# Performance work log

Measured on AMD Instinct MI355X. Metric: run time of the kernel, lower is better.

## Reference

```python
import jax, jax.numpy as jnp
import numpy as np

N_NODES = 16384
N_EDGES = 524288
N_GRAPHS = 256
IN_CH = 128
H_CH = 128   # per-head channels
HEADS = 2
LAYER_DIM = HEADS * H_CH  # 256, concat=True
POOL_DIM = 3 * LAYER_DIM  # 768
OUT_CH = 1
NEG_SLOPE = 0.2


def setup_inputs() -> dict:
    key = jax.random.key(0)
    ks = jax.random.split(key, 20)
    s = lambda k, shape, fan: jax.random.normal(k, shape, jnp.float32) * (1.0 / np.sqrt(fan))
    inp = {
        "x": jax.random.normal(ks[0], (N_NODES, IN_CH), jnp.float32),
        "edge_index": jax.random.randint(ks[1], (2, N_EDGES), 0, N_NODES, jnp.int64),
        "batch": jnp.sort(jax.random.randint(ks[2], (N_NODES,), 0, N_GRAPHS, jnp.int64)),
        # GATv2 layer 1 (in=128)
        "Wl1": s(ks[3], (IN_CH, LAYER_DIM), IN_CH), "Wr1": s(ks[4], (IN_CH, LAYER_DIM), IN_CH),
        "att1": s(ks[5], (HEADS, H_CH), H_CH), "b1": jnp.zeros((LAYER_DIM,), jnp.float32),
        # GATv2 layer 2 (in=256)
        "Wl2": s(ks[6], (LAYER_DIM, LAYER_DIM), LAYER_DIM), "Wr2": s(ks[7], (LAYER_DIM, LAYER_DIM), LAYER_DIM),
        "att2": s(ks[8], (HEADS, H_CH), H_CH), "b2": jnp.zeros((LAYER_DIM,), jnp.float32),
        # GATv2 layer 3 (in=256)
        "Wl3": s(ks[9], (LAYER_DIM, LAYER_DIM), LAYER_DIM), "Wr3": s(ks[10], (LAYER_DIM, LAYER_DIM), LAYER_DIM),
        "att3": s(ks[11], (HEADS, H_CH), H_CH), "b3": jnp.zeros((LAYER_DIM,), jnp.float32),
        # FFN (dropout inactive at eval)
        "fW1": s(ks[12], (POOL_DIM, POOL_DIM), POOL_DIM), "fb1": jnp.zeros((POOL_DIM,), jnp.float32),
        "fW2": s(ks[13], (POOL_DIM, OUT_CH), POOL_DIM), "fb2": jnp.zeros((OUT_CH,), jnp.float32),
    }
    return inp


def _gatv2(x, src, dst, Wl, Wr, att, b):
    """PyG GATv2Conv: per-edge score a . LeakyReLU(Wl x_src + Wr x_dst),
    softmax over incoming edges per destination, weighted scatter-add of Wl x_src."""
    n = x.shape[0]
    xl = (x @ Wl).reshape(n, HEADS, H_CH)  # source messages
    xr = (x @ Wr).reshape(n, HEADS, H_CH)  # target query
    e = jax.nn.leaky_relu(xl[src] + xr[dst], NEG_SLOPE)          # [E,H,C]
    logits = jnp.einsum('ehc,hc->eh', e, att)                    # [E,H]
    m = jax.ops.segment_max(logits, dst, num_segments=n)         # per-dst max (self-loops guarantee nonempty)
    ev = jnp.exp(logits - m[dst])
    denom = jax.ops.segment_sum(ev, dst, num_segments=n)
    alpha = ev / denom[dst]                                       # [E,H]
    out = jax.ops.segment_sum(alpha[..., None] * xl[src], dst, num_segments=n)  # [N,H,C]
    return out.reshape(n, LAYER_DIM) + b


def reference(x, edge_index, batch, Wl1, Wr1, att1, b1, Wl2, Wr2, att2, b2,
              Wl3, Wr3, att3, b3, fW1, fb1, fW2, fb2):
    n = x.shape[0]
    loops = jnp.arange(n, dtype=edge_index.dtype)
    src = jnp.concatenate([edge_index[0], loops])  # add_self_loops=True default
    dst = jnp.concatenate([edge_index[1], loops])
    h1 = _gatv2(x, src, dst, Wl1, Wr1, att1, b1)
    h2 = _gatv2(h1, src, dst, Wl2, Wr2, att2, b2)
    h3 = _gatv2(h2, src, dst, Wl3, Wr3, att3, b3)
    pool = lambda h: jax.ops.segment_sum(h, batch, num_segments=N_GRAPHS)
    h = jnp.concatenate([pool(h1), pool(h2), pool(h3)], axis=1)   # [G,768]
    h = jax.nn.relu(h @ fW1 + fb1)
    return h @ fW2 + fb2                                           # [G,1]
```

## Files before the change

### kernel.cpp

```cpp
#include <hip/hip_runtime.h>

#define NNODES 16384
#define NEDGES 524288
#define NETOT  (NEDGES + NNODES)
#define NGRAPH 256

typedef __attribute__((ext_vector_type(8))) short short8;
typedef __attribute__((ext_vector_type(4))) float f32x4;
typedef __attribute__((ext_vector_type(2))) float f32x2;

__device__ __forceinline__ float b2f(unsigned short u){
  union { unsigned int i; float f; } v; v.i = ((unsigned int)u) << 16; return v.f;
}
__device__ __forceinline__ unsigned short f2b(float f){
  union { float f; unsigned int i; } v; v.f = f;
  unsigned int r = v.i + 0x7FFFu + ((v.i >> 16) & 1u);
  return (unsigned short)(r >> 16);
}
__device__ __forceinline__ f32x2 unpack2(unsigned int u){
  union { unsigned int i; float f; } lo, hi;
  lo.i = u << 16; hi.i = u & 0xFFFF0000u;
  f32x2 r; r[0] = lo.f; r[1] = hi.f; return r;
}

__global__ void __launch_bounds__(256) zero_deg(int* __restrict__ deg){
  deg[blockIdx.x * 256 + threadIdx.x] = 0;
}

__global__ void __launch_bounds__(256) count_deg(const int* __restrict__ ei, int* __restrict__ deg){
  int i = blockIdx.x * 256 + threadIdx.x;
  int d = (i < NEDGES) ? ei[NEDGES + i] : (i - NEDGES);
  atomicAdd(&deg[d], 1);
}

__global__ void __launch_bounds__(256) scan1(const int* __restrict__ deg,
                                             int* __restrict__ incl, int* __restrict__ bsum){
  __shared__ int ws[4];
  const int b = blockIdx.x, t = threadIdx.x, lane = t & 63, w = t >> 6;
  int v = deg[b * 256 + t];
  int x = v;
  #pragma unroll
  for(int o = 1; o < 64; o <<= 1){ int u = __shfl_up(x, o, 64); if(lane >= o) x += u; }
  if(lane == 63) ws[w] = x;
  __syncthreads();
  int add = 0;
  #pragma unroll
  for(int j = 0; j < 4; j++) if(j < w) add += ws[j];
  incl[b * 256 + t] = x + add;
  if(t == 255) bsum[b] = x + add;
}

__global__ void __launch_bounds__(256) scan3(const int* __restrict__ deg, const int* __restrict__ incl,
                                             const int* __restrict__ bsum,
                                             int* __restrict__ row_off, int* __restrict__ cursor){
  __shared__ int boff_s;
  const int b = blockIdx.x, t = threadIdx.x;
  if(t < 64){
    int v = (t < b) ? bsum[t] : 0;
    #pragma unroll
    for(int o = 32; o > 0; o >>= 1) v += __shfl_xor(v, o, 64);
    if(t == 0) boff_s = v;
  }
  __syncthreads();
  const int i = b * 256 + t;
  int inc = incl[i] + boff_s;
  row_off[i + 1] = inc;
  cursor[i] = inc - deg[i];
  if(i == 0) row_off[0] = 0;
}

__global__ void __launch_bounds__(256) fill_csr(const int* __restrict__ ei, int* __restrict__ cursor,
                                                int* __restrict__ col_src){
  int i = blockIdx.x * 256 + threadIdx.x;
  int s, d;
  if(i < NEDGES){ s = ei[i]; d = ei[NEDGES + i]; }
  else          { s = i - NEDGES; d = s; }
  int p = atomicAdd(&cursor[d], 1);
  col_src[p] = s;
}

__global__ void __launch_bounds__(256) prep(const float* __restrict__ x,
                                            const float* __restrict__ Wl1, const float* __restrict__ Wr1,
                                            const float* __restrict__ Wl2, const float* __restrict__ Wr2,
                                            const float* __restrict__ Wl3, const float* __restrict__ Wr3,
                                            unsigned short* __restrict__ xb,
                                            unsigned short* __restrict__ Wt1,
                                            unsigned short* __restrict__ Wt2,
                                            unsigned short* __restrict__ Wt3){
  const int b = blockIdx.x, t = threadIdx.x;
  if(b < 8192){
    int i = b * 256 + t;
    xb[i] = f2b(x[i]);
    return;
  }
  const float *Wl, *Wr; unsigned short* Wt; int K, i;
  if(b < 8192 + 256){ Wl = Wl1; Wr = Wr1; Wt = Wt1; K = 128; i = (b - 8192) * 256 + t; }
  else if(b < 8192 + 256 + 512){ Wl = Wl2; Wr = Wr2; Wt = Wt2; K = 256; i = (b - 8448) * 256 + t; }
  else { Wl = Wl3; Wr = Wr3; Wt = Wt3; K = 256; i = (b - 8960) * 256 + t; }
  int k = i >> 9, c = i & 511;
  float val = (c < 256) ? Wl[(size_t)k * 256 + c] : Wr[(size_t)k * 256 + (c - 256)];
  Wt[(size_t)c * K + k] = f2b(val);
}

template<int K>
__global__ void __launch_bounds__(256) gemm_xw(const unsigned short* __restrict__ A,
                                               const unsigned short* __restrict__ Wt,
                                               unsigned short* __restrict__ Cout){
  __shared__ unsigned short As[128][40];
  __shared__ unsigned short Bs[128][40];
  const int t = threadIdx.x;
  const int rowbase = blockIdx.x * 128;
  const int colbase = blockIdx.y * 128;
  const int wave = t >> 6, lane = t & 63;
  const int lrow = lane & 15, kg = lane >> 4;

  f32x4 acc[2][8] = {};

  for(int kt = 0; kt < K; kt += 32){
    {
      int oct = t & 3, r = t >> 2;
      const unsigned short* ga = A + (size_t)(rowbase + r) * K + kt + oct * 8;
      short8 v0 = *(const short8*)ga;
      short8 v1 = *(const short8*)(ga + 64 * K);
      *(short8*)(&As[r][oct * 8])      = v0;
      *(short8*)(&As[r + 64][oct * 8]) = v1;
    }
    {
      int n = t & 127, kh = (t >> 7) * 16;
      const unsigned short* gw = Wt + (size_t)(colbase + n) * K + kt + kh;
      short8 v0 = *(const short8*)gw;
      short8 v1 = *(const short8*)(gw + 8);
      *(short8*)(&Bs[n][kh])     = v0;
      *(short8*)(&Bs[n][kh + 8]) = v1;
    }
    __syncthreads();
    short8 afrag[2], bfrag[8];
    afrag[0] = *(const short8*)(&As[wave * 32 + lrow][kg * 8]);
    afrag[1] = *(const short8*)(&As[wave * 32 + 16 + lrow][kg * 8]);
    #pragma unroll
    for(int fc = 0; fc < 8; fc++) bfrag[fc] = *(const short8*)(&Bs[fc * 16 + lrow][kg * 8]);
    #pragma unroll
    for(int rf = 0; rf < 2; rf++)
      #pragma unroll
      for(int fc = 0; fc < 8; fc++)
        acc[rf][fc] = __builtin_amdgcn_mfma_f32_16x16x32_bf16(afrag[rf], bfrag[fc], acc[rf][fc], 0, 0, 0);
    __syncthreads();
  }
  #pragma unroll
  for(int rf = 0; rf < 2; rf++)
    #pragma unroll
    for(int fc = 0; fc < 8; fc++)
      #pragma unroll
      for(int r = 0; r < 4; r++){
        int row = rowbase + wave * 32 + rf * 16 + kg * 4 + r;
        int col = colbase + fc * 16 + lrow;
        Cout[(size_t)row * 512 + col] = f2b(acc[rf][fc][r]);
      }
}

__global__ void __launch_bounds__(256) edge_agg(const unsigned short* __restrict__ xlb,
                                                const int* __restrict__ row_off,
                                                const int* __restrict__ col_src,
                                                const float* __restrict__ att,
                                                const float* __restrict__ bias,
                                                unsigned short* __restrict__ hout){
  const int n = (blockIdx.x * 256 + threadIdx.x) >> 6;
  const int lane = threadIdx.x & 63;
  const int eg = lane >> 4;
  const int c0 = (lane & 15) * 16;
  f32x2 xr[8], at[8];
  {
    const unsigned short* xp = xlb + (size_t)n * 512 + 256 + c0;
    uint4 v0 = *(const uint4*)xp;
    uint4 v1 = *(const uint4*)(xp + 8);
    xr[0] = unpack2(v0.x); xr[1] = unpack2(v0.y); xr[2] = unpack2(v0.z); xr[3] = unpack2(v0.w);
    xr[4] = unpack2(v1.x); xr[5] = unpack2(v1.y); xr[6] = unpack2(v1.z); xr[7] = unpack2(v1.w);
    #pragma unroll
    for(int i = 0; i < 8; i++) at[i] = *(const f32x2*)(att + c0 + 2 * i);
  }
  float s = 0.f;
  f32x2 ac[8] = {};
  const int beg = row_off[n], end = row_off[n + 1];
  for(int ch = beg; ch < end; ch += 64){
    int idx = ch + lane;
    int si = (idx < end) ? col_src[idx] : 0;
    int cnt = end - ch; if(cnt > 64) cnt = 64;
    for(int k = 0; k < cnt; k += 4){
      int kk = k + eg;
      int src = __shfl(si, kk);
      const unsigned short* gp = xlb + (size_t)src * 512 + c0;
      uint4 v0 = *(const uint4*)gp;
      uint4 v1 = *(const uint4*)(gp + 8);
      f32x2 x0 = unpack2(v0.x), x1 = unpack2(v0.y), x2 = unpack2(v0.z), x3 = unpack2(v0.w);
      f32x2 x4 = unpack2(v1.x), x5 = unpack2(v1.y), x6 = unpack2(v1.z), x7 = unpack2(v1.w);
      f32x2 e, p2;
      e = x0 + xr[0]; e = __builtin_elementwise_max(e, e * 0.2f); p2  = e * at[0];
      e = x1 + xr[1]; e = __builtin_elementwise_max(e, e * 0.2f); p2 += e * at[1];
      e = x2 + xr[2]; e = __builtin_elementwise_max(e, e * 0.2f); p2 += e * at[2];
      e = x3 + xr[3]; e = __builtin_elementwise_max(e, e * 0.2f); p2 += e * at[3];
      e = x4 + xr[4]; e = __builtin_elementwise_max(e, e * 0.2f); p2 += e * at[4];
      e = x5 + xr[5]; e = __builtin_elementwise_max(e, e * 0.2f); p2 += e * at[5];
      e = x6 + xr[6]; e = __builtin_elementwise_max(e, e * 0.2f); p2 += e * at[6];
      e = x7 + xr[7]; e = __builtin_elementwise_max(e, e * 0.2f); p2 += e * at[7];
      float p = p2[0] + p2[1];
      p += __shfl_xor(p, 1); p += __shfl_xor(p, 2); p += __shfl_xor(p, 4);
      float pe = (kk < cnt) ? __expf(p) : 0.f;
      s += pe;
      f32x2 pe2 = {pe, pe};
      ac[0] += pe2 * x0; ac[1] += pe2 * x1; ac[2] += pe2 * x2; ac[3] += pe2 * x3;
      ac[4] += pe2 * x4; ac[5] += pe2 * x5; ac[6] += pe2 * x6; ac[7] += pe2 * x7;
    }
  }
  s += __shfl_xor(s, 16); s += __shfl_xor(s, 32);
  #pragma unroll
  for(int i = 0; i < 8; i++){
    ac[i][0] += __shfl_xor(ac[i][0], 16); ac[i][0] += __shfl_xor(ac[i][0], 32);
    ac[i][1] += __shfl_xor(ac[i][1], 16); ac[i][1] += __shfl_xor(ac[i][1], 32);
  }
  if(eg == 0){
    float inv = 1.f / s;
    unsigned short o[16];
    #pragma unroll
    for(int i = 0; i < 8; i++){
      o[2 * i]     = f2b(fmaf(ac[i][0], inv, bias[c0 + 2 * i]));
      o[2 * i + 1] = f2b(fmaf(ac[i][1], inv, bias[c0 + 2 * i + 1]));
    }
    unsigned short* hp = hout + (size_t)n * 256 + c0;
    *(uint4*)hp       = *(const uint4*)&o[0];
    *(uint4*)(hp + 8) = *(const uint4*)&o[8];
  }
}

__device__ __forceinline__ int lbound(const int* __restrict__ a, int n, int v){
  int lo = 0, hi = n;
  while(lo < hi){ int mid = (lo + hi) >> 1; if(a[mid] < v) lo = mid + 1; else hi = mid; }
  return lo;
}

__global__ void __launch_bounds__(256) pool_accum(const unsigned short* __restrict__ h,
                                                  const int* __restrict__ batch,
                                                  float* __restrict__ pool, int slot){
  __shared__ float red[8][264];
  const int g = blockIdx.x, t = threadIdx.x;
  const int ng = t >> 5, c0 = (t & 31) * 8;
  const int lo = lbound(batch, NNODES, g);
  const int hi = lbound(batch, NNODES, g + 1);
  f32x2 a0 = {0.f,0.f}, a1 = {0.f,0.f}, a2 = {0.f,0.f}, a3 = {0.f,0.f};
  for(int node = lo + ng; node < hi; node += 8){
    uint4 v = *(const uint4*)(h + (size_t)node * 256 + c0);
    a0 += unpack2(v.x); a1 += unpack2(v.y); a2 += unpack2(v.z); a3 += unpack2(v.w);
  }
  red[ng][c0 + 0] = a0[0]; red[ng][c0 + 1] = a0[1];
  red[ng][c0 + 2] = a1[0]; red[ng][c0 + 3] = a1[1];
  red[ng][c0 + 4] = a2[0]; red[ng][c0 + 5] = a2[1];
  red[ng][c0 + 6] = a3[0]; red[ng][c0 + 7] = a3[1];
  __syncthreads();
  float s = 0.f;
  #pragma unroll
  for(int i = 0; i < 8; i++) s += red[i][t];
  pool[(size_t)g * 768 + slot * 256 + t] = s;
}

__global__ void __launch_bounds__(256) ffn1(const float* __restrict__ pool,
                                            const float* __restrict__ fW1,
                                            const float* __restrict__ fb1,
                                            float* __restrict__ hidden){
  __shared__ float ap[32][65];
  __shared__ float ws[64][33];
  const int t = threadIdx.x;
  const int cb = blockIdx.x * 32;
  const int gb = blockIdx.y * 32;
  const int tc = t & 31, tg = t >> 5;
  float acc[4] = {};
  for(int kc = 0; kc < 768; kc += 64){
    {
      int g_l = t >> 3, j8 = (t & 7) * 8;
      const float* gp = pool + (size_t)(gb + g_l) * 768 + kc + j8;
      #pragma unroll
      for(int i = 0; i < 8; i++) ap[g_l][j8 + i] = gp[i];
    }
    {
      int c_l = t & 31, k0 = (t >> 5) * 8;
      #pragma unroll
      for(int i = 0; i < 8; i++) ws[k0 + i][c_l] = fW1[(size_t)(kc + k0 + i) * 768 + cb + c_l];
    }
    __syncthreads();
    #pragma unroll
    for(int k = 0; k < 64; k++){
      float w = ws[k][tc];
      #pragma unroll
      for(int i = 0; i < 4; i++) acc[i] = fmaf(ap[tg * 4 + i][k], w, acc[i]);
    }
    __syncthreads();
  }
  float b = fb1[cb + tc];
  #pragma unroll
  for(int i = 0; i < 4; i++)
    hidden[(size_t)(gb + tg * 4 + i) * 768 + cb + tc] = fmaxf(acc[i] + b, 0.f);
}

__global__ void __launch_bounds__(256) ffn2(const float* __restrict__ hidden,
                                            const float* __restrict__ fW2,
                                            const float* __restrict__ fb2,
                                            float* __restrict__ out){
  const int g = (blockIdx.x * 256 + threadIdx.x) >> 6;
  const int lane = threadIdx.x & 63;
  float p = 0.f;
  for(int i = lane; i < 768; i += 64) p += hidden[(size_t)g * 768 + i] * fW2[i];
  #pragma unroll
  for(int o = 32; o > 0; o >>= 1) p += __shfl_xor(p, o, 64);
  if(lane == 0) out[g] = p + fb2[0];
}

extern "C" void kernel_launch(void* const* d_in, const int* in_sizes, int n_in,
                              void* d_out, int out_size, void* d_ws, size_t ws_size,
                              hipStream_t stream){
  const float* x    = (const float*)d_in[0];
  const int* ei     = (const int*)d_in[1];
  const int* batch  = (const int*)d_in[2];
  const float* Wl[3]  = {(const float*)d_in[3],  (const float*)d_in[7],  (const float*)d_in[11]};
  const float* Wr[3]  = {(const float*)d_in[4],  (const float*)d_in[8],  (const float*)d_in[12]};
  const float* att[3] = {(const float*)d_in[5],  (const float*)d_in[9],  (const float*)d_in[13]};
  const float* bp[3]  = {(const float*)d_in[6],  (const float*)d_in[10], (const float*)d_in[14]};
  const float* fW1 = (const float*)d_in[15];
  const float* fb1 = (const float*)d_in[16];
  const float* fW2 = (const float*)d_in[17];
  const float* fb2 = (const float*)d_in[18];

  char* ws = (char*)d_ws;
  size_t off = 0;
  auto alloc = [&](size_t sz){ size_t p = off; off += (sz + 255) & ~(size_t)255; return p; };
  int* deg      = (int*)(ws + alloc((size_t)NNODES * 4));
  int* rowoff   = (int*)(ws + alloc((size_t)(NNODES + 1) * 4));
  int* cursor   = (int*)(ws + alloc((size_t)NNODES * 4));
  int* colsrc   = (int*)(ws + alloc((size_t)NETOT * 4));
  int* incl     = (int*)(ws + alloc((size_t)NNODES * 4));
  int* bsum     = (int*)(ws + alloc(64 * 4));
  unsigned short* xb  = (unsigned short*)(ws + alloc((size_t)NNODES * 128 * 2));
  unsigned short* Wt1 = (unsigned short*)(ws + alloc((size_t)512 * 128 * 2));
  unsigned short* Wt2 = (unsigned short*)(ws + alloc((size_t)512 * 256 * 2));
  unsigned short* Wt3 = (unsigned short*)(ws + alloc((size_t)512 * 256 * 2));
  unsigned short* xlb = (unsigned short*)(ws + alloc((size_t)NNODES * 512 * 2));
  unsigned short* hA  = (unsigned short*)(ws + alloc((size_t)NNODES * 256 * 2));
  unsigned short* hB  = (unsigned short*)(ws + alloc((size_t)NNODES * 256 * 2));
  float* pool   = (float*)(ws + alloc((size_t)NGRAPH * 768 * 4));
  float* hidden = (float*)(ws + alloc((size_t)NGRAPH * 768 * 4));

  zero_deg<<<NNODES / 256, 256, 0, stream>>>(deg);
  count_deg<<<NETOT / 256, 256, 0, stream>>>(ei, deg);
  prep<<<8192 + 256 + 512 + 512, 256, 0, stream>>>(x, Wl[0], Wr[0], Wl[1], Wr[1], Wl[2], Wr[2],
                                                   xb, Wt1, Wt2, Wt3);
  scan1<<<NNODES / 256, 256, 0, stream>>>(deg, incl, bsum);
  scan3<<<NNODES / 256, 256, 0, stream>>>(deg, incl, bsum, rowoff, cursor);
  fill_csr<<<NETOT / 256, 256, 0, stream>>>(ei, cursor, colsrc);

  dim3 ggrid(NNODES / 128, 4);

  gemm_xw<128><<<ggrid, 256, 0, stream>>>(xb, Wt1, xlb);
  edge_agg<<<NNODES / 4, 256, 0, stream>>>(xlb, rowoff, colsrc, att[0], bp[0], hA);
  pool_accum<<<NGRAPH, 256, 0, stream>>>(hA, batch, pool, 0);

  gemm_xw<256><<<ggrid, 256, 0, stream>>>(hA, Wt2, xlb);
  edge_agg<<<NNODES / 4, 256, 0, stream>>>(xlb, rowoff, colsrc, att[1], bp[1], hB);
  pool_accum<<<NGRAPH, 256, 0, stream>>>(hB, batch, pool, 1);

  gemm_xw<256><<<ggrid, 256, 0, stream>>>(hB, Wt3, xlb);
  edge_agg<<<NNODES / 4, 256, 0, stream>>>(xlb, rowoff, colsrc, att[2], bp[2], hA);
  pool_accum<<<NGRAPH, 256, 0, stream>>>(hA, batch, pool, 2);

  ffn1<<<dim3(768 / 32, NGRAPH / 32), 256, 0, stream>>>(pool, fW1, fb1, hidden);
  ffn2<<<NGRAPH / 4, 256, 0, stream>>>(hidden, fW2, fb2, (float*)d_out);
}
```

Measured before the change: 286.3 us.

## Split GAT layers per head into compact buffers and fuse pooling into aggregation

The GEMM now writes xl for each head into its own compact 128-wide buffer and xr into a separate buffer. Edge aggregation runs once per head, so each gathered row is 256 bytes and the random-access footprint shrinks, which should improve L2 locality. Pooling is fused into edge_agg through float atomics, and the pool buffer is zeroed inside prep, which removes the pool_accum kernels. The change also adds a prefetch touch of the block's own xl rows, nontemporal loads and stores, and two edges per inner iteration. In exchange it doubles the number of aggregation launches and adds atomic contention on the pool buffer.

```diff
diff --git a/kernel.cpp b/kernel.cpp
--- a/kernel.cpp
+++ b/kernel.cpp
@@ -8,6 +8,7 @@
 typedef __attribute__((ext_vector_type(8))) short short8;
 typedef __attribute__((ext_vector_type(4))) float f32x4;
 typedef __attribute__((ext_vector_type(2))) float f32x2;
+typedef __attribute__((ext_vector_type(4))) unsigned int u32x4;
 
 __device__ __forceinline__ float b2f(unsigned short u){
   union { unsigned int i; float f; } v; v.i = ((unsigned int)u) << 16; return v.f;
@@ -86,11 +87,18 @@
                                             unsigned short* __restrict__ xb,
                                             unsigned short* __restrict__ Wt1,
                                             unsigned short* __restrict__ Wt2,
-                                            unsigned short* __restrict__ Wt3){
+                                            unsigned short* __restrict__ Wt3,
+                                            float* __restrict__ pool){
   const int b = blockIdx.x, t = threadIdx.x;
   if(b < 8192){
     int i = b * 256 + t;
     xb[i] = f2b(x[i]);
+    return;
+  }
+  if(b >= 9472){
+    int i = (b - 9472) * 1024 + t * 4;
+    f32x4 z = {0.f, 0.f, 0.f, 0.f};
+    *(f32x4*)(pool + i) = z;
     return;
   }
   const float *Wl, *Wr; unsigned short* Wt; int K, i;
@@ -105,12 +113,15 @@
 template<int K>
 __global__ void __launch_bounds__(256) gemm_xw(const unsigned short* __restrict__ A,
                                                const unsigned short* __restrict__ Wt,
-                                               unsigned short* __restrict__ Cout){
+                                               unsigned short* __restrict__ xl0,
+                                               unsigned short* __restrict__ xl1,
+                                               unsigned short* __restrict__ xr){
   __shared__ unsigned short As[128][40];
   __shared__ unsigned short Bs[128][40];
   const int t = threadIdx.x;
   const int rowbase = blockIdx.x * 128;
-  const int colbase = blockIdx.y * 128;
+  const int by = blockIdx.y;
+  const int colbase = by * 128;
   const int wave = t >> 6, lane = t & 63;
   const int lrow = lane & 15, kg = lane >> 4;
 
@@ -146,6 +157,10 @@
         acc[rf][fc] = __builtin_amdgcn_mfma_f32_16x16x32_bf16(afrag[rf], bfrag[fc], acc[rf][fc], 0, 0, 0);
     __syncthreads();
   }
+  unsigned short* outp; int stride, coloff;
+  if(by == 0){ outp = xl0; stride = 128; coloff = 0; }
+  else if(by == 1){ outp = xl1; stride = 128; coloff = 0; }
+  else { outp = xr; stride = 256; coloff = colbase - 256; }
   #pragma unroll
   for(int rf = 0; rf < 2; rf++)
     #pragma unroll
@@ -153,112 +168,100 @@
       #pragma unroll
       for(int r = 0; r < 4; r++){
         int row = rowbase + wave * 32 + rf * 16 + kg * 4 + r;
-        int col = colbase + fc * 16 + lrow;
-        Cout[(size_t)row * 512 + col] = f2b(acc[rf][fc][r]);
+        int col = coloff + fc * 16 + lrow;
+        outp[(size_t)row * stride + col] = f2b(acc[rf][fc][r]);
       }
 }
 
-__global__ void __launch_bounds__(256) edge_agg(const unsigned short* __restrict__ xlb,
+__global__ void __launch_bounds__(256) edge_agg(const unsigned short* __restrict__ xl,
+                                                const unsigned short* __restrict__ xr_o,
                                                 const int* __restrict__ row_off,
                                                 const int* __restrict__ col_src,
-                                                const float* __restrict__ att,
-                                                const float* __restrict__ bias,
-                                                unsigned short* __restrict__ hout){
+                                                const float* __restrict__ att_o,
+                                                const float* __restrict__ bias_o,
+                                                const int* __restrict__ batch,
+                                                unsigned short* __restrict__ hout_o,
+                                                float* __restrict__ pool_o){
   const int n = (blockIdx.x * 256 + threadIdx.x) >> 6;
   const int lane = threadIdx.x & 63;
   const int eg = lane >> 4;
-  const int c0 = (lane & 15) * 16;
-  f32x2 xr[8], at[8];
+  const int c0 = (lane & 15) * 8;
+
   {
-    const unsigned short* xp = xlb + (size_t)n * 512 + 256 + c0;
-    uint4 v0 = *(const uint4*)xp;
-    uint4 v1 = *(const uint4*)(xp + 8);
-    xr[0] = unpack2(v0.x); xr[1] = unpack2(v0.y); xr[2] = unpack2(v0.z); xr[3] = unpack2(v0.w);
-    xr[4] = unpack2(v1.x); xr[5] = unpack2(v1.y); xr[6] = unpack2(v1.z); xr[7] = unpack2(v1.w);
-    #pragma unroll
-    for(int i = 0; i < 8; i++) at[i] = *(const f32x2*)(att + c0 + 2 * i);
+    const unsigned short* wbase = xl + ((size_t)(blockIdx.x >> 3) << 12);
+    u32x4 d0 = *(const u32x4*)(wbase + threadIdx.x * 8);
+    u32x4 d1 = *(const u32x4*)(wbase + 2048 + threadIdx.x * 8);
+    asm volatile("" :: "v"(d0), "v"(d1));
+  }
+
+  f32x2 xr[4], at[4];
+  {
+    u32x4 v = __builtin_nontemporal_load((const u32x4*)(xr_o + (size_t)n * 256 + c0));
+    xr[0] = unpack2(v.x); xr[1] = unpack2(v.y); xr[2] = unpack2(v.z); xr[3] = unpack2(v.w);
+    #pragma unroll
+    for(int i = 0; i < 4; i++) at[i] = *(const f32x2*)(att_o + c0 + 2 * i);
   }
   float s = 0.f;
-  f32x2 ac[8] = {};
+  f32x2 ac[4] = {};
   const int beg = row_off[n], end = row_off[n + 1];
   for(int ch = beg; ch < end; ch += 64){
     int idx = ch + lane;
-    int si = (idx < end) ? col_src[idx] : 0;
+    int si = (idx < end) ? __builtin_nontemporal_load(col_src + idx) : 0;
     int cnt = end - ch; if(cnt > 64) cnt = 64;
-    for(int k = 0; k < cnt; k += 4){
-      int kk = k + eg;
-      int src = __shfl(si, kk);
-      const unsigned short* gp = xlb + (size_t)src * 512 + c0;
-      uint4 v0 = *(const uint4*)gp;
-      uint4 v1 = *(const uint4*)(gp + 8);
-      f32x2 x0 = unpack2(v0.x), x1 = unpack2(v0.y), x2 = unpack2(v0.z), x3 = unpack2(v0.w);
-      f32x2 x4 = unpack2(v1.x), x5 = unpack2(v1.y), x6 = unpack2(v1.z), x7 = unpack2(v1.w);
-      f32x2 e, p2;
-      e = x0 + xr[0]; e = __builtin_elementwise_max(e, e * 0.2f); p2  = e * at[0];
-      e = x1 + xr[1]; e = __builtin_elementwise_max(e, e * 0.2f); p2 += e * at[1];
-      e = x2 + xr[2]; e = __builtin_elementwise_max(e, e * 0.2f); p2 += e * at[2];
-      e = x3 + xr[3]; e = __builtin_elementwise_max(e, e * 0.2f); p2 += e * at[3];
-      e = x4 + xr[4]; e = __builtin_elementwise_max(e, e * 0.2f); p2 += e * at[4];
-      e = x5 + xr[5]; e = __builtin_elementwise_max(e, e * 0.2f); p2 += e * at[5];
-      e = x6 + xr[6]; e = __builtin_elementwise_max(e, e * 0.2f); p2 += e * at[6];
-      e = x7 + xr[7]; e = __builtin_elementwise_max(e, e * 0.2f); p2 += e * at[7];
-      float p = p2[0] + p2[1];
-      p += __shfl_xor(p, 1); p += __shfl_xor(p, 2); p += __shfl_xor(p, 4);
-      float pe = (kk < cnt) ? __expf(p) : 0.f;
-      s += pe;
-      f32x2 pe2 = {pe, pe};
-      ac[0] += pe2 * x0; ac[1] += pe2 * x1; ac[2] += pe2 * x2; ac[3] += pe2 * x3;
-      ac[4] += pe2 * x4; ac[5] += pe2 * x5; ac[6] += pe2 * x6; ac[7] += pe2 * x7;
+    for(int k = 0; k < cnt; k += 8){
+      int ka = k + eg, kb = k + 4 + eg;
+      int srcA = __shfl(si, ka), srcB = __shfl(si, kb);
+      u32x4 va = *(const u32x4*)(xl + (size_t)srcA * 128 + c0);
+      u32x4 vb = *(const u32x4*)(xl + (size_t)srcB * 128 + c0);
+      f32x2 a0 = unpack2(va.x), a1 = unpack2(va.y), a2 = unpack2(va.z), a3 = unpack2(va.w);
+      f32x2 b0 = unpack2(vb.x), b1 = unpack2(vb.y), b2 = unpack2(vb.z), b3 = unpack2(vb.w);
+      f32x2 e, pa2, pb2;
+      e = a0 + xr[0]; e = __builtin_elementwise_max(e, e * 0.2f); pa2  = e * at[0];
+      e = a1 + xr[1]; e = __builtin_elementwise_max(e, e * 0.2f); pa2 += e * at[1];
+      e = a2 + xr[2]; e = __builtin_elementwise_max(e, e * 0.2f); pa2 += e * at[2];
+      e = a3 + xr[3]; e = __builtin_elementwise_max(e, e * 0.2f); pa2 += e * at[3];
+      e = b0 + xr[0]; e = __builtin_elementwise_max(e, e * 0.2f); pb2  = e * at[0];
+      e = b1 + xr[1]; e = __builtin_elementwise_max(e, e * 0.2f); pb2 += e * at[1];
+      e = b2 + xr[2]; e = __builtin_elementwise_max(e, e * 0.2f); pb2 += e * at[2];
+      e = b3 + xr[3]; e = __builtin_elementwise_max(e, e * 0.2f); pb2 += e * at[3];
+      float pa = pa2[0] + pa2[1], pb = pb2[0] + pb2[1];
+      pa += __shfl_xor(pa, 1); pb += __shfl_xor(pb, 1);
+      pa += __shfl_xor(pa, 2); pb += __shfl_xor(pb, 2);
+      pa += __shfl_xor(pa, 4); pb += __shfl_xor(pb, 4);
+      pa += __shfl_xor(pa, 8); pb += __shfl_xor(pb, 8);
+      float pea = (ka < cnt) ? __expf(pa) : 0.f;
+      float peb = (kb < cnt) ? __expf(pb) : 0.f;
+      s += pea + peb;
+      f32x2 va2 = {pea, pea}, vb2 = {peb, peb};
+      ac[0] += va2 * a0 + vb2 * b0;
+      ac[1] += va2 * a1 + vb2 * b1;
+      ac[2] += va2 * a2 + vb2 * b2;
+      ac[3] += va2 * a3 + vb2 * b3;
     }
   }
   s += __shfl_xor(s, 16); s += __shfl_xor(s, 32);
   #pragma unroll
-  for(int i = 0; i < 8; i++){
+  for(int i = 0; i < 4; i++){
     ac[i][0] += __shfl_xor(ac[i][0], 16); ac[i][0] += __shfl_xor(ac[i][0], 32);
     ac[i][1] += __shfl_xor(ac[i][1], 16); ac[i][1] += __shfl_xor(ac[i][1], 32);
   }
   if(eg == 0){
     float inv = 1.f / s;
-    unsigned short o[16];
-    #pragma unroll
-    for(int i = 0; i < 8; i++){
-      o[2 * i]     = f2b(fmaf(ac[i][0], inv, bias[c0 + 2 * i]));
-      o[2 * i + 1] = f2b(fmaf(ac[i][1], inv, bias[c0 + 2 * i + 1]));
-    }
-    unsigned short* hp = hout + (size_t)n * 256 + c0;
-    *(uint4*)hp       = *(const uint4*)&o[0];
-    *(uint4*)(hp + 8) = *(const uint4*)&o[8];
-  }
-}
-
-__device__ __forceinline__ int lbound(const int* __restrict__ a, int n, int v){
-  int lo = 0, hi = n;
-  while(lo < hi){ int mid = (lo + hi) >> 1; if(a[mid] < v) lo = mid + 1; else hi = mid; }
-  return lo;
-}
-
-__global__ void __launch_bounds__(256) pool_accum(const unsigned short* __restrict__ h,
-                                                  const int* __restrict__ batch,
-                                                  float* __restrict__ pool, int slot){
-  __shared__ float red[8][264];
-  const int g = blockIdx.x, t = threadIdx.x;
-  const int ng = t >> 5, c0 = (t & 31) * 8;
-  const int lo = lbound(batch, NNODES, g);
-  const int hi = lbound(batch, NNODES, g + 1);
-  f32x2 a0 = {0.f,0.f}, a1 = {0.f,0.f}, a2 = {0.f,0.f}, a3 = {0.f,0.f};
-  for(int node = lo + ng; node < hi; node += 8){
-    uint4 v = *(const uint4*)(h + (size_t)node * 256 + c0);
-    a0 += unpack2(v.x); a1 += unpack2(v.y); a2 += unpack2(v.z); a3 += unpack2(v.w);
-  }
-  red[ng][c0 + 0] = a0[0]; red[ng][c0 + 1] = a0[1];
-  red[ng][c0 + 2] = a1[0]; red[ng][c0 + 3] = a1[1];
-  red[ng][c0 + 4] = a2[0]; red[ng][c0 + 5] = a2[1];
-  red[ng][c0 + 6] = a3[0]; red[ng][c0 + 7] = a3[1];
-  __syncthreads();
-  float s = 0.f;
-  #pragma unroll
-  for(int i = 0; i < 8; i++) s += red[i][t];
-  pool[(size_t)g * 768 + slot * 256 + t] = s;
+    float o[8];
+    #pragma unroll
+    for(int i = 0; i < 4; i++){
+      o[2 * i]     = fmaf(ac[i][0], inv, bias_o[c0 + 2 * i]);
+      o[2 * i + 1] = fmaf(ac[i][1], inv, bias_o[c0 + 2 * i + 1]);
+    }
+    unsigned short ob[8];
+    #pragma unroll
+    for(int i = 0; i < 8; i++) ob[i] = f2b(o[i]);
+    __builtin_nontemporal_store(*(const u32x4*)ob, (u32x4*)(hout_o + (size_t)n * 256 + c0));
+    int g = __builtin_nontemporal_load(batch + n);
+    float* pp = pool_o + (size_t)g * 768 + c0;
+    #pragma unroll
+    for(int i = 0; i < 8; i++) atomicAdd(pp + i, o[i]);
+  }
 }
 
 __global__ void __launch_bounds__(256) ffn1(const float* __restrict__ pool,
@@ -340,7 +343,9 @@
   unsigned short* Wt1 = (unsigned short*)(ws + alloc((size_t)512 * 128 * 2));
   unsigned short* Wt2 = (unsigned short*)(ws + alloc((size_t)512 * 256 * 2));
   unsigned short* Wt3 = (unsigned short*)(ws + alloc((size_t)512 * 256 * 2));
-  unsigned short* xlb = (unsigned short*)(ws + alloc((size_t)NNODES * 512 * 2));
+  unsigned short* xl0 = (unsigned short*)(ws + alloc((size_t)NNODES * 128 * 2));
+  unsigned short* xl1 = (unsigned short*)(ws + alloc((size_t)NNODES * 128 * 2));
+  unsigned short* xr  = (unsigned short*)(ws + alloc((size_t)NNODES * 256 * 2));
   unsigned short* hA  = (unsigned short*)(ws + alloc((size_t)NNODES * 256 * 2));
   unsigned short* hB  = (unsigned short*)(ws + alloc((size_t)NNODES * 256 * 2));
   float* pool   = (float*)(ws + alloc((size_t)NGRAPH * 768 * 4));
@@ -348,25 +353,29 @@
 
   zero_deg<<<NNODES / 256, 256, 0, stream>>>(deg);
   count_deg<<<NETOT / 256, 256, 0, stream>>>(ei, deg);
-  prep<<<8192 + 256 + 512 + 512, 256, 0, stream>>>(x, Wl[0], Wr[0], Wl[1], Wr[1], Wl[2], Wr[2],
-                                                   xb, Wt1, Wt2, Wt3);
+  prep<<<8192 + 256 + 512 + 512 + 192, 256, 0, stream>>>(x, Wl[0], Wr[0], Wl[1], Wr[1], Wl[2], Wr[2],
+                                                         xb, Wt1, Wt2, Wt3, pool);
   scan1<<<NNODES / 256, 256, 0, stream>>>(deg, incl, bsum);
   scan3<<<NNODES / 256, 256, 0, stream>>>(deg, incl, bsum, rowoff, cursor);
   fill_csr<<<NETOT / 256, 256, 0, stream>>>(ei, cursor, colsrc);
 
   dim3 ggrid(NNODES / 128, 4);
-
-  gemm_xw<128><<<ggrid, 256, 0, stream>>>(xb, Wt1, xlb);
-  edge_agg<<<NNODES / 4, 256, 0, stream>>>(xlb, rowoff, colsrc, att[0], bp[0], hA);
-  pool_accum<<<NGRAPH, 256, 0, stream>>>(hA, batch, pool, 0);
-
-  gemm_xw<256><<<ggrid, 256, 0, stream>>>(hA, Wt2, xlb);
-  edge_agg<<<NNODES / 4, 256, 0, stream>>>(xlb, rowoff, colsrc, att[1], bp[1], hB);
-  pool_accum<<<NGRAPH, 256, 0, stream>>>(hB, batch, pool, 1);
-
-  gemm_xw<256><<<ggrid, 256, 0, stream>>>(hB, Wt3, xlb);
-  edge_agg<<<NNODES / 4, 256, 0, stream>>>(xlb, rowoff, colsrc, att[2], bp[2], hA);
-  pool_accum<<<NGRAPH, 256, 0, stream>>>(hA, batch, pool, 2);
+  const int EAG = NNODES / 4;
+
+  unsigned short* hbuf[3] = {hA, hB, hA};
+  const unsigned short* abuf[3] = {xb, hA, hB};
+  unsigned short* wbuf[3] = {Wt1, Wt2, Wt3};
+
+  for(int L = 0; L < 3; L++){
+    if(L == 0) gemm_xw<128><<<ggrid, 256, 0, stream>>>(abuf[0], wbuf[0], xl0, xl1, xr);
+    else       gemm_xw<256><<<ggrid, 256, 0, stream>>>(abuf[L], wbuf[L], xl0, xl1, xr);
+    for(int H = 0; H < 2; H++){
+      const unsigned short* xl = H ? xl1 : xl0;
+      edge_agg<<<EAG, 256, 0, stream>>>(xl, xr + H * 128, rowoff, colsrc,
+                                        att[L] + H * 128, bp[L] + H * 128, batch,
+                                        hbuf[L] + H * 128, pool + L * 256 + H * 128);
+    }
+  }
 
   ffn1<<<dim3(768 / 32, NGRAPH / 32), 256, 0, stream>>>(pool, fW1, fb1, hidden);
   ffn2<<<NGRAPH / 4, 256, 0, stream>>>(hidden, fW2, fb2, (float*)d_out);
```

After: 784.3 us. +173.9%, slower.
